# Kernel tuning notes

Hardware: AMD Instinct MI355X
Metric: run time of the kernel (lower is better)

## Reference

```python
import jax, jax.numpy as jnp
import numpy as np

MARGIN = 0.3
NEG_INF = jnp.float32(-1e30)


def setup_inputs() -> dict:
    key = jax.random.key(0)
    k1, k2 = jax.random.split(key)
    features = jax.random.normal(k1, (8192, 128), dtype=jnp.float32)
    labels = jax.random.randint(k2, (8192,), 0, 512)
    return {"features": features, "labels": labels}


def reference(features, labels):
    n = features.shape[0]
    # pairwise Euclidean distance, clamped like the torch code
    x2 = jnp.sum(features * features, axis=1, keepdims=True)          # [N,1]
    d2 = x2 + x2.T - 2.0 * (features @ features.T)                    # [N,N]
    dist = jnp.sqrt(jnp.clip(d2, 1e-8))

    same = labels[None, :] == labels[:, None]                          # [N,N]
    eye = jnp.eye(n, dtype=bool)
    pos_mask = same & ~eye                                             # positives, self excluded
    neg_mask = ~same

    # soft mining: softmax-weighted positive distance (weights ~ softmax(d))
    pos_logits = jnp.where(pos_mask, dist, NEG_INF)
    pw = jax.nn.softmax(pos_logits, axis=1)
    wp = jnp.sum(pw * jnp.where(pos_mask, dist, 0.0), axis=1)          # [N]

    # softmax-weighted negative distance (weights ~ softmax(-d))
    neg_logits = jnp.where(neg_mask, -dist, NEG_INF)
    nw = jax.nn.softmax(neg_logits, axis=1)
    wn = jnp.sum(nw * jnp.where(neg_mask, dist, 0.0), axis=1)          # [N]

    # soft margin: softplus(diff + margin)
    loss = jax.nn.softplus(wp - wn + MARGIN)

    # rows without any positive or any negative are skipped in the original
    valid = pos_mask.any(axis=1) & neg_mask.any(axis=1)
    loss = jnp.where(valid, loss, 0.0)
    denom = jnp.maximum(jnp.sum(valid.astype(jnp.float32)), 1.0)
    return jnp.sum(loss) / denom
```

## Files before the change

kernel.cpp:

```cpp
#include <hip/hip_runtime.h>
#include <hip/hip_bf16.h>


typedef __bf16 bf16x8 __attribute__((ext_vector_type(8)));
typedef float f32x4 __attribute__((ext_vector_type(4)));

#define NROWS 8192
#define DIM 128
#define JTILE 64
#define LDS_STRIDE 136
#define MARGIN_F 0.3f
#define SQRT2_F 1.41421356f

__global__ __launch_bounds__(256) void prep_kernel(const float* __restrict__ F,
                                                   __hip_bfloat16* __restrict__ Fb,
                                                   float* __restrict__ x2,
                                                   float* __restrict__ gstat) {
    const int tid = threadIdx.x;
    const int wave = tid >> 6, lane = tid & 63;
    const int row = blockIdx.x * 4 + wave;
    float2 f = ((const float2*)(F + (size_t)row * DIM))[lane];
    ((__hip_bfloat162*)(Fb + (size_t)row * DIM))[lane] = __float22bfloat162_rn(f);
    float ss = f.x * f.x + f.y * f.y;
#pragma unroll
    for (int m = 32; m > 0; m >>= 1) ss += __shfl_xor(ss, m, 64);
    if (lane == 0) x2[row] = ss;
    if (blockIdx.x == 0 && tid < 2) gstat[tid] = 0.f;
}

__global__ __launch_bounds__(256, 6) void pairs_kernel(
        const __hip_bfloat16* __restrict__ Fb,
        const float* __restrict__ x2,
        const int* __restrict__ labels,
        float4* __restrict__ partial,
        int jspan) {
    __shared__ __hip_bfloat16 sB[JTILE * LDS_STRIDE];
    __shared__ int sLab[JTILE];
    __shared__ float sX2h[JTILE];

    const int tid = threadIdx.x;
    const int wave = tid >> 6;
    const int lane = tid & 63;
    const int quad = lane >> 4;
    const int lm = lane & 15;
    const int rbase = blockIdx.x * 64 + wave * 16;

    bf16x8 a[4];
#pragma unroll
    for (int kc = 0; kc < 4; ++kc)
        a[kc] = *(const bf16x8*)(Fb + (size_t)(rbase + lm) * DIM + kc * 32 + quad * 8);

    int ig[4]; float x2ih[4]; int labi[4];
#pragma unroll
    for (int r = 0; r < 4; ++r) {
        ig[r] = rbase + quad * 4 + r;
        x2ih[r] = -0.5f * x2[ig[r]];
        labi[r] = labels[ig[r]];
    }

    float nl4[4] = {0,0,0,0}, ns4[4] = {0,0,0,0};
    float pl4[4] = {0,0,0,0}, ps4[4] = {0,0,0,0};

    const int j0 = blockIdx.y * jspan;
    const int jiters = jspan / JTILE;

    for (int jb = 0; jb < jiters; ++jb) {
        const int jbase = j0 + jb * JTILE;
        __syncthreads();
#pragma unroll
        for (int s = 0; s < 4; ++s) {
            int c = tid + s * 256;
            int jr = c >> 4, ck = c & 15;
            *(bf16x8*)(sB + jr * LDS_STRIDE + ck * 8) =
                *(const bf16x8*)(Fb + (size_t)(jbase + jr) * DIM + ck * 8);
        }
        if (tid < JTILE) {
            sLab[tid] = labels[jbase + tid];
            sX2h[tid] = -0.5f * x2[jbase + tid];
        }
        __syncthreads();

#pragma unroll
        for (int jt = 0; jt < 4; ++jt) {
            const int jl = jt * 16 + lm;
            const __hip_bfloat16* bp = sB + jl * LDS_STRIDE + quad * 8;
            const float xjh = sX2h[jl];
            f32x4 acc;
#pragma unroll
            for (int r = 0; r < 4; ++r) acc[r] = x2ih[r] + xjh;
#pragma unroll
            for (int kc = 0; kc < 4; ++kc) {
                bf16x8 b = *(const bf16x8*)(bp + kc * 32);
                acc = __builtin_amdgcn_mfma_f32_16x16x32_bf16(a[kc], b, acc, 0, 0, 0);
            }
            const int labj = sLab[jl];
            const int jglob = jbase + jl;
#pragma unroll
            for (int r = 0; r < 4; ++r) {
                float d2h = fmaxf(-acc[r], 5e-9f);
                float s = __builtin_amdgcn_sqrtf(d2h);
                float ne = __expf(-SQRT2_F * s);
                bool same = (labj == labi[r]);
                float mne = same ? 0.f : ne;
                nl4[r] += mne;
                ns4[r] = fmaf(mne, s, ns4[r]);
                if (same && (jglob != ig[r])) {
                    float pe = __expf(fmaf(SQRT2_F, s, -30.f));
                    pl4[r] += pe;
                    ps4[r] = fmaf(pe, s, ps4[r]);
                }
            }
        }
    }

#pragma unroll
    for (int m = 1; m < 16; m <<= 1) {
#pragma unroll
        for (int r = 0; r < 4; ++r) {
            pl4[r] += __shfl_xor(pl4[r], m, 64);
            ps4[r] += __shfl_xor(ps4[r], m, 64);
            nl4[r] += __shfl_xor(nl4[r], m, 64);
            ns4[r] += __shfl_xor(ns4[r], m, 64);
        }
    }
    if (lm == 0) {
#pragma unroll
        for (int r = 0; r < 4; ++r)
            partial[(size_t)blockIdx.y * NROWS + ig[r]] =
                make_float4(pl4[r], ps4[r], nl4[r], ns4[r]);
    }
}

__global__ __launch_bounds__(256) void finalize_kernel(const float4* __restrict__ partial,
                                                       float* __restrict__ gstat,
                                                       int jsplit) {
    const int row = blockIdx.x * 256 + threadIdx.x;
    float pl = 0.f, ps = 0.f, nl = 0.f, ns = 0.f;
    for (int s = 0; s < jsplit; ++s) {
        float4 p = partial[(size_t)s * NROWS + row];
        pl += p.x; ps += p.y; nl += p.z; ns += p.w;
    }
    float sum = 0.f, cnt = 0.f;
    if (pl > 0.f && nl > 0.f) {
        float x = fmaf(SQRT2_F, ps / pl - ns / nl, MARGIN_F);
        sum = fmaxf(x, 0.f) + log1pf(__expf(-fabsf(x)));
        cnt = 1.f;
    }
#pragma unroll
    for (int m = 32; m > 0; m >>= 1) {
        sum += __shfl_xor(sum, m, 64);
        cnt += __shfl_xor(cnt, m, 64);
    }
    __shared__ float sS[4], sC[4];
    const int wave = threadIdx.x >> 6, lane = threadIdx.x & 63;
    if (lane == 0) { sS[wave] = sum; sC[wave] = cnt; }
    __syncthreads();
    if (threadIdx.x == 0) {
        unsafeAtomicAdd(&gstat[0], sS[0] + sS[1] + sS[2] + sS[3]);
        unsafeAtomicAdd(&gstat[1], sC[0] + sC[1] + sC[2] + sC[3]);
    }
}

__global__ void div_kernel(const float* __restrict__ gstat, float* __restrict__ out) {
    out[0] = gstat[0] / fmaxf(gstat[1], 1.0f);
}

extern "C" void kernel_launch(void* const* d_in, const int* in_sizes, int n_in,
                              void* d_out, int out_size, void* d_ws, size_t ws_size,
                              hipStream_t stream) {
    const float* F = (const float*)d_in[0];
    const int* labels = (const int*)d_in[1];
    float* out = (float*)d_out;

    char* ws = (char*)d_ws;
    __hip_bfloat16* Fb = (__hip_bfloat16*)ws;
    size_t off = (size_t)NROWS * DIM * 2;
    float* x2 = (float*)(ws + off);  off += (size_t)NROWS * 4;
    float4* partial = (float4*)(ws + off);

    int jsplit = 16;
    while (jsplit > 1 && off + (size_t)jsplit * NROWS * 16 + 16 > ws_size) jsplit >>= 1;
    float* gstat = (float*)(ws + off + (size_t)jsplit * NROWS * 16);

    prep_kernel<<<NROWS / 4, 256, 0, stream>>>(F, Fb, x2, gstat);
    pairs_kernel<<<dim3(NROWS / 64, jsplit), 256, 0, stream>>>(Fb, x2, labels, partial,
                                                               NROWS / jsplit);
    finalize_kernel<<<NROWS / 256, 256, 0, stream>>>(partial, gstat, jsplit);
    div_kernel<<<1, 1, 0, stream>>>(gstat, out);
}
```

Before: 125.1 us.

## Drop label checks from pair loop and correct same-label pairs in a per-label kernel

The main pairwise kernel now sums negative-softmax terms over all columns, with no label comparison and no positive branch. A new per-label kernel gathers the members of each label and computes positive sums along with the same-label negative contributions, which are subtracted later. This lightens the hot inner loop and allows higher occupancy. The divide kernel is folded into finalize using a last-block atomic counter. Risks: group capacity is capped at 64 members per label (assumes small classes), and subtracting large terms can cancel catastrophically.

```diff
diff --git a/kernel.cpp b/kernel.cpp
--- a/kernel.cpp
+++ b/kernel.cpp
@@ -9,12 +9,18 @@
 #define DIM 128
 #define JTILE 64
 #define LDS_STRIDE 136
+#define NLABELS 512
+#define GCAP 64
 #define MARGIN_F 0.3f
 #define SQRT2_F 1.41421356f
+#define K1F (-2.04027892f)
+#define K2F ( 2.04027892f)
+#define C2F (-43.2808512f)
 
 __global__ __launch_bounds__(256) void prep_kernel(const float* __restrict__ F,
                                                    __hip_bfloat16* __restrict__ Fb,
                                                    float* __restrict__ x2,
+                                                   float4* __restrict__ corr,
                                                    float* __restrict__ gstat) {
     const int tid = threadIdx.x;
     const int wave = tid >> 6, lane = tid & 63;
@@ -25,17 +31,49 @@
 #pragma unroll
     for (int m = 32; m > 0; m >>= 1) ss += __shfl_xor(ss, m, 64);
     if (lane == 0) x2[row] = ss;
-    if (blockIdx.x == 0 && tid < 2) gstat[tid] = 0.f;
-}
-
-__global__ __launch_bounds__(256, 6) void pairs_kernel(
+    const int g = blockIdx.x * 256 + tid;
+    if (g < NROWS) corr[g] = make_float4(0.f, 0.f, 0.f, 0.f);
+    if (blockIdx.x == 0 && tid < 4) gstat[tid] = 0.f;
+}
+
+template<bool DIAG>
+__device__ __forceinline__ void tile_body(const __hip_bfloat16* __restrict__ sB,
+                                          const float* __restrict__ sX2h,
+                                          const bf16x8* a, const float* x2ih,
+                                          float (&nl4)[4], float (&ns4)[4],
+                                          int lm, int quad, int ig0, int jbase) {
+#pragma unroll
+    for (int jt = 0; jt < 4; ++jt) {
+        const int jl = jt * 16 + lm;
+        const __hip_bfloat16* bp = sB + jl * LDS_STRIDE + quad * 8;
+        const float xjh = sX2h[jl];
+        f32x4 acc;
+#pragma unroll
+        for (int r = 0; r < 4; ++r) acc[r] = x2ih[r] + xjh;
+#pragma unroll
+        for (int kc = 0; kc < 4; ++kc) {
+            bf16x8 b = *(const bf16x8*)(bp + kc * 32);
+            acc = __builtin_amdgcn_mfma_f32_16x16x32_bf16(a[kc], b, acc, 0, 0, 0);
+        }
+        const int dj = jbase + jl - ig0;
+#pragma unroll
+        for (int r = 0; r < 4; ++r) {
+            float d2h = fmaxf(-acc[r], 5e-9f);
+            float s = __builtin_amdgcn_sqrtf(d2h);
+            float ne = __builtin_amdgcn_exp2f(K1F * s);
+            if (DIAG) ne = (dj == r) ? 0.f : ne;
+            nl4[r] += ne;
+            ns4[r] = fmaf(ne, s, ns4[r]);
+        }
+    }
+}
+
+__global__ __launch_bounds__(256, 8) void pairs_kernel(
         const __hip_bfloat16* __restrict__ Fb,
         const float* __restrict__ x2,
-        const int* __restrict__ labels,
-        float4* __restrict__ partial,
+        float2* __restrict__ partial,
         int jspan) {
     __shared__ __hip_bfloat16 sB[JTILE * LDS_STRIDE];
-    __shared__ int sLab[JTILE];
     __shared__ float sX2h[JTILE];
 
     const int tid = threadIdx.x;
@@ -50,19 +88,16 @@
     for (int kc = 0; kc < 4; ++kc)
         a[kc] = *(const bf16x8*)(Fb + (size_t)(rbase + lm) * DIM + kc * 32 + quad * 8);
 
-    int ig[4]; float x2ih[4]; int labi[4];
-#pragma unroll
-    for (int r = 0; r < 4; ++r) {
-        ig[r] = rbase + quad * 4 + r;
-        x2ih[r] = -0.5f * x2[ig[r]];
-        labi[r] = labels[ig[r]];
-    }
+    const int ig0 = rbase + quad * 4;
+    float x2ih[4];
+#pragma unroll
+    for (int r = 0; r < 4; ++r) x2ih[r] = -0.5f * x2[ig0 + r];
 
     float nl4[4] = {0,0,0,0}, ns4[4] = {0,0,0,0};
-    float pl4[4] = {0,0,0,0}, ps4[4] = {0,0,0,0};
 
     const int j0 = blockIdx.y * jspan;
-    const int jiters = jspan / JTILE;
+    const int jiters = jspan >> 6;
+    const int djb = blockIdx.x - blockIdx.y * jiters;
 
     for (int jb = 0; jb < jiters; ++jb) {
         const int jbase = j0 + jb * JTILE;
@@ -74,51 +109,19 @@
             *(bf16x8*)(sB + jr * LDS_STRIDE + ck * 8) =
                 *(const bf16x8*)(Fb + (size_t)(jbase + jr) * DIM + ck * 8);
         }
-        if (tid < JTILE) {
-            sLab[tid] = labels[jbase + tid];
-            sX2h[tid] = -0.5f * x2[jbase + tid];
-        }
+        if (tid < JTILE) sX2h[tid] = -0.5f * x2[jbase + tid];
         __syncthreads();
 
-#pragma unroll
-        for (int jt = 0; jt < 4; ++jt) {
-            const int jl = jt * 16 + lm;
-            const __hip_bfloat16* bp = sB + jl * LDS_STRIDE + quad * 8;
-            const float xjh = sX2h[jl];
-            f32x4 acc;
-#pragma unroll
-            for (int r = 0; r < 4; ++r) acc[r] = x2ih[r] + xjh;
-#pragma unroll
-            for (int kc = 0; kc < 4; ++kc) {
-                bf16x8 b = *(const bf16x8*)(bp + kc * 32);
-                acc = __builtin_amdgcn_mfma_f32_16x16x32_bf16(a[kc], b, acc, 0, 0, 0);
-            }
-            const int labj = sLab[jl];
-            const int jglob = jbase + jl;
-#pragma unroll
-            for (int r = 0; r < 4; ++r) {
-                float d2h = fmaxf(-acc[r], 5e-9f);
-                float s = __builtin_amdgcn_sqrtf(d2h);
-                float ne = __expf(-SQRT2_F * s);
-                bool same = (labj == labi[r]);
-                float mne = same ? 0.f : ne;
-                nl4[r] += mne;
-                ns4[r] = fmaf(mne, s, ns4[r]);
-                if (same && (jglob != ig[r])) {
-                    float pe = __expf(fmaf(SQRT2_F, s, -30.f));
-                    pl4[r] += pe;
-                    ps4[r] = fmaf(pe, s, ps4[r]);
-                }
-            }
-        }
+        if (jb == djb)
+            tile_body<true >(sB, sX2h, a, x2ih, nl4, ns4, lm, quad, ig0, jbase);
+        else
+            tile_body<false>(sB, sX2h, a, x2ih, nl4, ns4, lm, quad, ig0, jbase);
     }
 
 #pragma unroll
     for (int m = 1; m < 16; m <<= 1) {
 #pragma unroll
         for (int r = 0; r < 4; ++r) {
-            pl4[r] += __shfl_xor(pl4[r], m, 64);
-            ps4[r] += __shfl_xor(ps4[r], m, 64);
             nl4[r] += __shfl_xor(nl4[r], m, 64);
             ns4[r] += __shfl_xor(ns4[r], m, 64);
         }
@@ -126,23 +129,102 @@
     if (lm == 0) {
 #pragma unroll
         for (int r = 0; r < 4; ++r)
-            partial[(size_t)blockIdx.y * NROWS + ig[r]] =
-                make_float4(pl4[r], ps4[r], nl4[r], ns4[r]);
-    }
-}
-
-__global__ __launch_bounds__(256) void finalize_kernel(const float4* __restrict__ partial,
+            partial[(size_t)blockIdx.y * NROWS + ig0 + r] =
+                make_float2(nl4[r], ns4[r]);
+    }
+}
+
+__global__ __launch_bounds__(64) void corr_kernel(
+        const __hip_bfloat16* __restrict__ Fb,
+        const float* __restrict__ x2,
+        const int* __restrict__ labels,
+        float4* __restrict__ corr) {
+    const int L = blockIdx.x;
+    const int lane = threadIdx.x;
+    __shared__ int sIdx[GCAP];
+
+    int cnt = 0;
+    for (int c0 = 0; c0 < NROWS; c0 += 256) {
+        int4 lv = *(const int4*)(labels + c0 + lane * 4);
+#pragma unroll
+        for (int k = 0; k < 4; ++k) {
+            int labk = (k == 0) ? lv.x : (k == 1) ? lv.y : (k == 2) ? lv.z : lv.w;
+            unsigned long long m = __ballot(labk == L);
+            while (m) {
+                int b = __builtin_ctzll(m);
+                m &= m - 1;
+                if (lane == 0 && cnt < GCAP) sIdx[cnt] = c0 + b * 4 + k;
+                ++cnt;
+            }
+        }
+    }
+    const int gsz = cnt < GCAP ? cnt : GCAP;
+    if (gsz == 0) return;
+    __syncthreads();
+
+    const int b4 = lane >> 2;
+    const int cc = lane & 3;
+
+    for (int aI = 0; aI < gsz; ++aI) {
+        const int ia = sIdx[aI];
+        const __hip_bfloat16* pa = Fb + (size_t)ia * DIM + cc * 32;
+        bf16x8 areg[4];
+#pragma unroll
+        for (int u = 0; u < 4; ++u) areg[u] = ((const bf16x8*)pa)[u];
+        const float x2ha = 0.5f * x2[ia];
+
+        float nl = 0.f, ns = 0.f, pl = 0.f, ps = 0.f;
+        for (int bb = 0; bb < gsz; bb += 16) {
+            const int b = bb + b4;
+            const bool bv = (b < gsz) && (b != aI);
+            const int ib = sIdx[b < gsz ? b : gsz - 1];
+            const __hip_bfloat16* pb = Fb + (size_t)ib * DIM + cc * 32;
+            float dot = 0.f;
+#pragma unroll
+            for (int u = 0; u < 4; ++u) {
+                bf16x8 breg = ((const bf16x8*)pb)[u];
+#pragma unroll
+                for (int e = 0; e < 8; ++e)
+                    dot = fmaf((float)areg[u][e], (float)breg[e], dot);
+            }
+            dot += __shfl_xor(dot, 1, 64);
+            dot += __shfl_xor(dot, 2, 64);
+            const float x2hb = 0.5f * x2[ib];
+            float d2h = fmaxf(x2ha + x2hb - dot, 5e-9f);
+            float s = __builtin_amdgcn_sqrtf(d2h);
+            float ne = __builtin_amdgcn_exp2f(K1F * s);
+            float pe = __builtin_amdgcn_exp2f(fmaf(K2F, s, C2F));
+            if (bv && cc == 0) {
+                nl += ne; ns = fmaf(ne, s, ns);
+                pl += pe; ps = fmaf(pe, s, ps);
+            }
+        }
+#pragma unroll
+        for (int m = 4; m < 64; m <<= 1) {
+            nl += __shfl_xor(nl, m, 64);
+            ns += __shfl_xor(ns, m, 64);
+            pl += __shfl_xor(pl, m, 64);
+            ps += __shfl_xor(ps, m, 64);
+        }
+        if (lane == 0) corr[ia] = make_float4(pl, ps, -nl, -ns);
+    }
+}
+
+__global__ __launch_bounds__(256) void finalize_kernel(const float2* __restrict__ partial,
+                                                       const float4* __restrict__ corr,
                                                        float* __restrict__ gstat,
+                                                       float* __restrict__ out,
                                                        int jsplit) {
     const int row = blockIdx.x * 256 + threadIdx.x;
-    float pl = 0.f, ps = 0.f, nl = 0.f, ns = 0.f;
+    float4 c = corr[row];
+    float nl = c.z, ns = c.w;
     for (int s = 0; s < jsplit; ++s) {
-        float4 p = partial[(size_t)s * NROWS + row];
-        pl += p.x; ps += p.y; nl += p.z; ns += p.w;
+        float2 p = partial[(size_t)s * NROWS + row];
+        nl += p.x; ns += p.y;
     }
     float sum = 0.f, cnt = 0.f;
-    if (pl > 0.f && nl > 0.f) {
-        float x = fmaf(SQRT2_F, ps / pl - ns / nl, MARGIN_F);
+    if (c.x > 0.f && nl > 0.f) {
+        float x = fmaf(SQRT2_F, c.y / c.x - ns / nl, MARGIN_F);
         sum = fmaxf(x, 0.f) + log1pf(__expf(-fabsf(x)));
         cnt = 1.f;
     }
@@ -158,11 +240,14 @@
     if (threadIdx.x == 0) {
         unsafeAtomicAdd(&gstat[0], sS[0] + sS[1] + sS[2] + sS[3]);
         unsafeAtomicAdd(&gstat[1], sC[0] + sC[1] + sC[2] + sC[3]);
-    }
-}
-
-__global__ void div_kernel(const float* __restrict__ gstat, float* __restrict__ out) {
-    out[0] = gstat[0] / fmaxf(gstat[1], 1.0f);
+        __threadfence();
+        unsigned t = atomicAdd((unsigned int*)(gstat + 2), 1u);
+        if (t == (unsigned)(gridDim.x - 1)) {
+            float s2 = unsafeAtomicAdd(&gstat[0], 0.f);
+            float c2 = unsafeAtomicAdd(&gstat[1], 0.f);
+            out[0] = s2 / fmaxf(c2, 1.f);
+        }
+    }
 }
 
 extern "C" void kernel_launch(void* const* d_in, const int* in_sizes, int n_in,
@@ -176,15 +261,16 @@
     __hip_bfloat16* Fb = (__hip_bfloat16*)ws;
     size_t off = (size_t)NROWS * DIM * 2;
     float* x2 = (float*)(ws + off);  off += (size_t)NROWS * 4;
-    float4* partial = (float4*)(ws + off);
+    float4* corr = (float4*)(ws + off);  off += (size_t)NROWS * 16;
 
     int jsplit = 16;
-    while (jsplit > 1 && off + (size_t)jsplit * NROWS * 16 + 16 > ws_size) jsplit >>= 1;
-    float* gstat = (float*)(ws + off + (size_t)jsplit * NROWS * 16);
-
-    prep_kernel<<<NROWS / 4, 256, 0, stream>>>(F, Fb, x2, gstat);
-    pairs_kernel<<<dim3(NROWS / 64, jsplit), 256, 0, stream>>>(Fb, x2, labels, partial,
+    while (jsplit > 1 && off + (size_t)jsplit * NROWS * 8 + 16 > ws_size) jsplit >>= 1;
+    float2* partial = (float2*)(ws + off);
+    float* gstat = (float*)(ws + off + (size_t)jsplit * NROWS * 8);
+
+    prep_kernel<<<NROWS / 4, 256, 0, stream>>>(F, Fb, x2, corr, gstat);
+    pairs_kernel<<<dim3(NROWS / 64, jsplit), 256, 0, stream>>>(Fb, x2, labels ? partial : partial,
                                                                NROWS / jsplit);
-    finalize_kernel<<<NROWS / 256, 256, 0, stream>>>(partial, gstat, jsplit);
-    div_kernel<<<1, 1, 0, stream>>>(gstat, out);
-}
+    corr_kernel<<<NLABELS, 64, 0, stream>>>(Fb, x2, labels, corr);
+    finalize_kernel<<<NROWS / 256, 256, 0, stream>>>(partial, corr, gstat, out, jsplit);
+}
```

Result: slower. 213.4 us (+70.6%).
